# Performance work log

Hardware: AMD Instinct MI355X
Metric: run time of the kernel (lower is better)

The kernel has to match this reference:

```python
import jax, jax.numpy as jnp
import numpy as np

# LIFNeuronFDE constants (from init_kwargs)
TAU = 0.5          # membrane time constant (tau_learnable=False)
THRESH = 1.0       # firing threshold V_th
SCALE = 5.0        # surrogate steepness
BETA = 0.5         # fractional order
H = 1.0            # step size h
T, B, N = 32, 32, 32768


def setup_inputs() -> dict:
    key = jax.random.key(0)
    k1, k2 = jax.random.split(key)
    I = jax.random.normal(k1, (T, B, N), dtype=jnp.float32)
    v0 = 0.1 * jax.random.normal(k2, (B, N), dtype=jnp.float32)
    return {"I": I, "v0": v0}


def _gl_coeffs(T_steps: int, beta: float) -> jnp.ndarray:
    # c_0 = 1, c_j = (1 - (1+beta)/j) * c_{j-1}  -> length T+1
    j = np.arange(1, T_steps + 1, dtype=np.float64)
    c = np.concatenate([[1.0], np.cumprod(1.0 - (1.0 + beta) / j)])
    return jnp.asarray(c, dtype=jnp.float32)


def reference(I, v0):
    # Fractional-order LIF with Grunwald-Letnikov memory:
    #   v^{k+1} = h^beta * (-v^k + I^k)/tau - sum_{j=0}^{k} c_{k+1-j} v^{(j)}
    #   spike   = sigmoid(scale * (v - V_th))   (continuous surrogate spike)
    Tn = I.shape[0]
    c = _gl_coeffs(Tn, BETA)                       # (T+1,)
    h_beta = jnp.float32(H ** BETA)
    jidx = jnp.arange(Tn)                          # history slot indices

    def step(carry, I_k):
        v, hist, k = carry                         # hist: (T, B, N)
        hist = hist.at[k].set(v)                   # store v^{(k)} in history buffer
        # coefficient c_{k+1-j} applied to v^{(j)} for j <= k; 0 for unwritten slots
        w = jnp.where(jidx <= k, jnp.take(c, jnp.clip(k + 1 - jidx, 0, Tn)), 0.0)
        mem_sum = jnp.einsum('t,tbn->bn', w, hist)  # GL memory term
        v_next = h_beta * (-v + I_k) / TAU - mem_sum
        spike = jax.nn.sigmoid(SCALE * (v_next - THRESH))
        return (v_next, hist, k + 1), spike

    hist0 = jnp.zeros((Tn,) + v0.shape, v0.dtype)
    _, spikes = jax.lax.scan(step, (v0, hist0, jnp.int32(0)), I)
    return spikes  # (T, B, N) continuous spike outputs
```

## Files before the change

### kernel.cpp

```cpp
#include <hip/hip_runtime.h>
#include <math.h>


#define T_STEPS 32
#define BN (32 * 32768)
#define PAIRS (BN / 2)

struct LinMap {
    double a[T_STEPS][T_STEPS];
    double b[T_STEPS];
};

constexpr LinMap make_linmap() {
    double c[T_STEPS + 1] = {};
    c[0] = 1.0;
    for (int j = 1; j <= T_STEPS; ++j) c[j] = c[j - 1] * (1.0 - 1.5 / (double)j);

    double vc[T_STEPS + 1][T_STEPS + 1] = {};
    vc[0][0] = 1.0;

    LinMap r{};
    for (int k = 0; k < T_STEPS; ++k) {
        for (int m = 0; m <= T_STEPS; ++m) {
            double acc = -2.0 * vc[k][m];
            for (int j = 0; j <= k; ++j) acc -= c[k + 1 - j] * vc[j][m];
            vc[k + 1][m] = acc;
        }
        vc[k + 1][1 + k] += 2.0;

        r.b[k] = vc[k + 1][0];
        for (int j = 0; j < T_STEPS; ++j) r.a[k][j] = vc[k + 1][1 + j];
    }
    return r;
}

constexpr LinMap CM = make_linmap();

template<int K>
__device__ __forceinline__ void fde_rows(const float2 (&If)[T_STEPS],
                                         const double v0x, const double v0y,
                                         float2* __restrict__ out2,
                                         const int idx)
{
    if constexpr (K < T_STEPS) {
        double sx = CM.b[K] * v0x;
        double sy = CM.b[K] * v0y;
        #pragma unroll
        for (int j = 0; j <= K; ++j) {
            sx = fma(CM.a[K][j], (double)If[j].x, sx);
            sy = fma(CM.a[K][j], (double)If[j].y, sy);
        }
        const float ax = (float)(-5.0 * (sx - 1.0));
        const float ay = (float)(-5.0 * (sy - 1.0));
        out2[(size_t)K * PAIRS + idx] =
            make_float2(1.0f / (1.0f + __expf(ax)), 1.0f / (1.0f + __expf(ay)));

        fde_rows<K + 1>(If, v0x, v0y, out2, idx);
    }
}

__global__ __launch_bounds__(256) void lif_fde_kernel(
    const float* __restrict__ I,
    const float* __restrict__ v0,
    float* __restrict__ out)
{
    const int idx = blockIdx.x * blockDim.x + threadIdx.x;

    const float2* __restrict__ I2   = (const float2*)I;
    const float2* __restrict__ v02  = (const float2*)v0;
    float2* __restrict__       out2 = (float2*)out;

    float2 If[T_STEPS];
    #pragma unroll
    for (int k = 0; k < T_STEPS; ++k) {
        If[k] = I2[(size_t)k * PAIRS + idx];
    }

    const float2 v0f = v02[idx];
    const double v0x = (double)v0f.x;
    const double v0y = (double)v0f.y;

    fde_rows<0>(If, v0x, v0y, out2, idx);
}

extern "C" void kernel_launch(void* const* d_in, const int* in_sizes, int n_in,
                              void* d_out, int out_size, void* d_ws, size_t ws_size,
                              hipStream_t stream) {
    const float* I  = (const float*)d_in[0];
    const float* v0 = (const float*)d_in[1];
    float* out = (float*)d_out;

    dim3 block(256);
    dim3 grid(PAIRS / 256);
    lif_fde_kernel<<<grid, block, 0, stream>>>(I, v0, out);
}
```

Before: 55.74 us.

## Split output rows into three blocks and stage input loads across them

Restructures the per-thread computation from a gather, where each output row sums over all prior inputs, into a scatter over three row blocks. The first two thirds of the input loads are issued up front and the last third is deferred until after the first block is computed, so loads overlap with FP64 math. It also replaces the float division in the sigmoid with the hardware reciprocal intrinsic. Keeping up to 64 double accumulators live risks higher register pressure and lower occupancy, and the reciprocal is slightly less accurate.

```diff
diff --git a/kernel.cpp b/kernel.cpp
--- a/kernel.cpp
+++ b/kernel.cpp
@@ -5,6 +5,8 @@
 #define T_STEPS 32
 #define BN (32 * 32768)
 #define PAIRS (BN / 2)
+#define RB1 11
+#define RB2 22
 
 struct LinMap {
     double a[T_STEPS][T_STEPS];
@@ -27,7 +29,6 @@
             vc[k + 1][m] = acc;
         }
         vc[k + 1][1 + k] += 2.0;
-
         r.b[k] = vc[k + 1][0];
         for (int j = 0; j < T_STEPS; ++j) r.a[k][j] = vc[k + 1][1 + j];
     }
@@ -36,26 +37,44 @@
 
 constexpr LinMap CM = make_linmap();
 
-template<int K>
-__device__ __forceinline__ void fde_rows(const float2 (&If)[T_STEPS],
-                                         const double v0x, const double v0y,
-                                         float2* __restrict__ out2,
-                                         const int idx)
+template<int J0, int J1>
+__device__ __forceinline__ void stage(float2 (&If)[T_STEPS],
+                                      const float2* __restrict__ I2, const int idx)
 {
-    if constexpr (K < T_STEPS) {
-        double sx = CM.b[K] * v0x;
-        double sy = CM.b[K] * v0y;
+    #pragma unroll
+    for (int j = J0; j < J1; ++j) If[j] = I2[(size_t)j * PAIRS + idx];
+}
+
+template<int K0, int KEND>
+__device__ __forceinline__ void init_s(double (&sx)[T_STEPS], double (&sy)[T_STEPS],
+                                       const double v0x, const double v0y)
+{
+    #pragma unroll
+    for (int k = K0; k < KEND; ++k) { sx[k] = CM.b[k] * v0x; sy[k] = CM.b[k] * v0y; }
+}
+
+template<int J, int K0, int KEND>
+__device__ __forceinline__ void scatter_phase(const float2 (&If)[T_STEPS],
+                                              double (&sx)[T_STEPS], double (&sy)[T_STEPS],
+                                              float2* __restrict__ out2, const int idx)
+{
+    if constexpr (J < KEND) {
+        const double Ix = (double)If[J].x;
+        const double Iy = (double)If[J].y;
+        constexpr int kst = (J > K0) ? J : K0;
         #pragma unroll
-        for (int j = 0; j <= K; ++j) {
-            sx = fma(CM.a[K][j], (double)If[j].x, sx);
-            sy = fma(CM.a[K][j], (double)If[j].y, sy);
+        for (int k = kst; k < KEND; ++k) {
+            sx[k] = fma(CM.a[k][J], Ix, sx[k]);
+            sy[k] = fma(CM.a[k][J], Iy, sy[k]);
         }
-        const float ax = (float)(-5.0 * (sx - 1.0));
-        const float ay = (float)(-5.0 * (sy - 1.0));
-        out2[(size_t)K * PAIRS + idx] =
-            make_float2(1.0f / (1.0f + __expf(ax)), 1.0f / (1.0f + __expf(ay)));
-
-        fde_rows<K + 1>(If, v0x, v0y, out2, idx);
+        if constexpr (J >= K0) {
+            const float ax = (float)(-5.0 * (sx[J] - 1.0));
+            const float ay = (float)(-5.0 * (sy[J] - 1.0));
+            out2[(size_t)J * PAIRS + idx] =
+                make_float2(__builtin_amdgcn_rcpf(1.0f + __expf(ax)),
+                            __builtin_amdgcn_rcpf(1.0f + __expf(ay)));
+        }
+        scatter_phase<J + 1, K0, KEND>(If, sx, sy, out2, idx);
     }
 }
 
@@ -71,16 +90,25 @@
     float2* __restrict__       out2 = (float2*)out;
 
     float2 If[T_STEPS];
-    #pragma unroll
-    for (int k = 0; k < T_STEPS; ++k) {
-        If[k] = I2[(size_t)k * PAIRS + idx];
-    }
+    double sx[T_STEPS], sy[T_STEPS];
+
+    stage<0, RB1>(If, I2, idx);
+    stage<RB1, RB2>(If, I2, idx);
 
     const float2 v0f = v02[idx];
     const double v0x = (double)v0f.x;
     const double v0y = (double)v0f.y;
 
-    fde_rows<0>(If, v0x, v0y, out2, idx);
+    init_s<0, RB1>(sx, sy, v0x, v0y);
+    scatter_phase<0, 0, RB1>(If, sx, sy, out2, idx);
+
+    stage<RB2, T_STEPS>(If, I2, idx);
+
+    init_s<RB1, RB2>(sx, sy, v0x, v0y);
+    scatter_phase<0, RB1, RB2>(If, sx, sy, out2, idx);
+
+    init_s<RB2, T_STEPS>(sx, sy, v0x, v0y);
+    scatter_phase<0, RB2, T_STEPS>(If, sx, sy, out2, idx);
 }
 
 extern "C" void kernel_launch(void* const* d_in, const int* in_sizes, int n_in,
```

Result: no change. 55.91 us (+0.3%).
